# Optimization experiments

Measured on AMD Instinct MI355X. Metric: run time of the kernel, lower is better.

## Reference

```python
import jax, jax.numpy as jnp
import numpy as np

B = 32768
IN_DIM, OUT_DIM, VAR_DIM = 2, 3, 50
KER_DIMS = [1024, 1024, 1024, 1024]
NSTEPS = 32  # fixed-step RK4 stand-in for adaptive odeint over t in [0, 1]


def setup_inputs() -> dict:
    key = jax.random.key(0)
    ks = jax.random.split(key, 11)
    x = jax.random.normal(ks[0], (B, IN_DIM), dtype=jnp.float32)
    dims = [VAR_DIM] + KER_DIMS + [VAR_DIM]
    inp = {"x": x}
    for i, (d1, d2) in enumerate(zip(dims[:-1], dims[1:])):
        # torch Linear(d1+1, d2): weight (d2, d1+1); stored here as (d1+1, d2)
        bound = 1.0 / np.sqrt(d1 + 1)
        inp[f"W{i}"] = jax.random.uniform(ks[1 + 2 * i], (d1 + 1, d2), jnp.float32, -bound, bound)
        inp[f"b{i}"] = jax.random.uniform(ks[2 + 2 * i], (d2,), jnp.float32, -bound, bound)
    return inp


def _odefunc(t, y, Ws, bs):
    # Each layer: concat time column, Linear, ReLU (except last) -- matches ODEfunc.forward
    out = y
    n = len(Ws)
    for i in range(n):
        tcol = jnp.full((out.shape[0], 1), t, dtype=out.dtype)
        h = jnp.concatenate([out, tcol], axis=1)
        out = h @ Ws[i] + bs[i]
        if i < n - 1:
            out = jax.nn.relu(out)
    return out


def _integrate(x, Ws, bs):
    # Pad input into var_dim state: out[:, :in_dim] = x, rest zeros
    y0 = jnp.zeros((x.shape[0], VAR_DIM), dtype=x.dtype).at[:, : x.shape[1]].set(x)
    dt = jnp.asarray(1.0 / NSTEPS, dtype=x.dtype)
    ts = jnp.arange(NSTEPS, dtype=x.dtype) * dt

    def step(y, t):
        k1 = _odefunc(t, y, Ws, bs)
        k2 = _odefunc(t + dt * 0.5, y + dt * 0.5 * k1, Ws, bs)
        k3 = _odefunc(t + dt * 0.5, y + dt * 0.5 * k2, Ws, bs)
        k4 = _odefunc(t + dt, y + dt * k3, Ws, bs)
        return y + (dt / 6.0) * (k1 + 2.0 * k2 + 2.0 * k3 + k4), None

    y1, _ = jax.lax.scan(step, y0, ts)
    return y1[:, :OUT_DIM]


def reference(x, W0, b0, W1, b1, W2, b2, W3, b3, W4, b4):
    Ws = (W0, W1, W2, W3, W4)
    bs = (b0, b1, b2, b3, b4)
    return _integrate(x, Ws, bs)
```

## Files before the change

kernel.cpp:

```cpp
#include <hip/hip_runtime.h>
#include <hip/hip_bf16.h>
#include <stdint.h>


typedef __bf16 bf16_t;
typedef bf16_t bf16x8 __attribute__((ext_vector_type(8)));
typedef float  f32x4  __attribute__((ext_vector_type(4)));

#define DEVI static __device__ __forceinline__

DEVI void gload_lds16(const bf16_t* gsrc, bf16_t* ldst) {
  __builtin_amdgcn_global_load_lds(
      (const __attribute__((address_space(1))) uint32_t*)gsrc,
      (__attribute__((address_space(3))) uint32_t*)ldst,
      16, 0, 0);
}

template<int K>
__global__ __launch_bounds__(512, 2) void gemm256(
    const bf16_t* __restrict__ A,
    const bf16_t* __restrict__ BT,
    const float* __restrict__ bias,
    const float* __restrict__ wtime,
    float t,
    bf16_t* __restrict__ C, int ldc,
    int M, int N)
{
  constexpr int NT = K / 64;
  static_assert(NT >= 2, "need >=2 K-tiles");

  __shared__ __align__(16) bf16_t As[2][256][64];
  __shared__ __align__(16) bf16_t Bs[2][256][64];

  const int tid  = threadIdx.x;
  const int wave = tid >> 6;
  const int lane = tid & 63;
  const int wr = wave >> 2;
  const int wc = wave & 3;

  int wg = blockIdx.x;
  {
    const int cpx = gridDim.x >> 3;
    wg = (wg & 7) * cpx + (wg >> 3);
  }
  const int nbn = N >> 8;
  const int bm = (wg / nbn) << 8;
  const int bn = (wg % nbn) << 8;

  const int srow = lane >> 3;
  const int scol = ((lane & 7) << 3) ^ ((lane & 32) >> 1);
  const bf16_t* aS = A  + (size_t)(bm + wave * 8 + srow) * K + scol;
  const bf16_t* bS = BT + (size_t)(bn + wave * 8 + srow) * K + scol;
  bf16_t* aD = &As[0][0][0] + wave * 8 * 64;
  bf16_t* bD = &Bs[0][0][0] + wave * 8 * 64;

  auto stage = [&](int g) {
    if (g >= 4 * NT) return;
    const int kt   = g >> 2;
    const int idx  = g & 3;
    const int hoff = (idx >> 1) << 7;
    const int buf  = kt & 1;
    const bf16_t* src = (idx & 1) ? bS : aS;
    bf16_t*       dst = (idx & 1) ? bD : aD;
    src += (size_t)hoff * K + kt * 64;
    dst += (buf * 256 + hoff) * 64;
    gload_lds16(src,                dst);
    gload_lds16(src + (size_t)64*K, dst + 64 * 64);
  };

  const int fr = lane & 15;
  const int fq = lane >> 4;

  bf16x8 af[8];
  bf16x8 bfr[8];
  f32x4  acc[8][4] = {};

  auto lda_frag = [&](int buf, int mh) {
    const char* base = (const char*)&As[buf][0][0];
#pragma unroll
    for (int m = 0; m < 4; ++m)
#pragma unroll
      for (int kk = 0; kk < 2; ++kk) {
        int r  = wr * 128 + (mh * 4 + m) * 16 + fr;
        int cb = (kk * 64 + fq * 16) ^ ((r & 4) << 3);
        af[m * 2 + kk] = *(const bf16x8*)(base + r * 128 + cb);
      }
  };
  auto ldb_frag = [&](int buf, int nh) {
    const char* base = (const char*)&Bs[buf][0][0];
#pragma unroll
    for (int n = 0; n < 2; ++n)
#pragma unroll
      for (int kk = 0; kk < 2; ++kk) {
        int r  = wc * 64 + (nh * 2 + n) * 16 + fr;
        int cb = (kk * 64 + fq * 16) ^ ((r & 4) << 3);
        bfr[nh * 4 + n * 2 + kk] = *(const bf16x8*)(base + r * 128 + cb);
      }
  };
  auto mma_quad = [&](int mh, int nh) {
    __builtin_amdgcn_s_setprio(1);
#pragma unroll
    for (int m = 0; m < 4; ++m)
#pragma unroll
      for (int n = 0; n < 2; ++n)
#pragma unroll
        for (int kk = 0; kk < 2; ++kk)
          acc[mh * 4 + m][nh * 2 + n] = __builtin_amdgcn_mfma_f32_16x16x32_bf16(
              af[m * 2 + kk], bfr[nh * 4 + n * 2 + kk],
              acc[mh * 4 + m][nh * 2 + n], 0, 0, 0);
    __builtin_amdgcn_s_setprio(0);
  };

#pragma unroll
  for (int g = 0; g < 7; ++g) stage(g);
  asm volatile("s_waitcnt vmcnt(6)" ::: "memory");
  __builtin_amdgcn_s_barrier();

  for (int t2 = 0; t2 < NT; ++t2) {
    const int buf = t2 & 1;
    const int gb  = t2 * 4 + 7;
    lda_frag(buf, 0);
    ldb_frag(buf, 0);
    stage(gb + 0);
    asm volatile("s_waitcnt lgkmcnt(8)" ::: "memory");
    __builtin_amdgcn_s_barrier();
    asm volatile("s_waitcnt lgkmcnt(0)" ::: "memory");
    mma_quad(0, 0);
    __builtin_amdgcn_s_barrier();
    ldb_frag(buf, 1);
    stage(gb + 1);
    __builtin_amdgcn_s_barrier();
    asm volatile("s_waitcnt lgkmcnt(0)" ::: "memory");
    mma_quad(0, 1);
    __builtin_amdgcn_s_barrier();
    lda_frag(buf, 1);
    stage(gb + 2);
    __builtin_amdgcn_s_barrier();
    asm volatile("s_waitcnt lgkmcnt(0)" ::: "memory");
    mma_quad(1, 0);
    __builtin_amdgcn_s_barrier();
    stage(gb + 3);
    if (t2 < NT - 2) asm volatile("s_waitcnt vmcnt(6)" ::: "memory");
    else             asm volatile("s_waitcnt vmcnt(0)" ::: "memory");
    __builtin_amdgcn_s_barrier();
    mma_quad(1, 1);
    __builtin_amdgcn_s_barrier();
  }

#pragma unroll
  for (int n = 0; n < 4; ++n) {
    const int gcol = bn + wc * 64 + n * 16 + fr;
    const float bv = bias[gcol] + t * wtime[gcol];
#pragma unroll
    for (int m = 0; m < 8; ++m) {
      const int grow0 = bm + wr * 128 + m * 16 + (fq << 2);
#pragma unroll
      for (int r = 0; r < 4; ++r) {
        float v = acc[m][n][r] + bv;
        v = v > 0.0f ? v : 0.0f;
        C[(size_t)(grow0 + r) * ldc + gcol] = (bf16_t)v;
      }
    }
  }
}

template<int BM, int BN, int BK, int WROWS, int WCOLS, bool RELU, bool OUT_BF16>
__global__ __launch_bounds__(256) void gemm_bt(
    const bf16_t* __restrict__ A, int lda,
    const bf16_t* __restrict__ BT,
    const float* __restrict__ bias,
    const float* __restrict__ wtime,
    float t,
    void* __restrict__ Cv, int ldc,
    int M, int K)
{
  constexpr int MR  = BM / WROWS / 16;
  constexpr int NR  = BN / WCOLS / 16;
  constexpr int TPR = BK / 8;
  constexpr int RPW = 64 / TPR;
  constexpr int RPL = 4 * RPW;
  static_assert(BM % RPL == 0 && BN % RPL == 0, "tile staging mismatch");

  __shared__ bf16_t As[BM][BK];
  __shared__ bf16_t Bs[BN][BK];

  const int tid  = threadIdx.x;
  const int wave = tid >> 6;
  const int lane = tid & 63;
  const int wr = wave / WCOLS;
  const int wc = wave % WCOLS;
  const int bm = blockIdx.x * BM;
  const int bn = blockIdx.y * BN;
  const int lrow = lane / TPR;
  const int lcol = (lane % TPR) * 8;

  f32x4 acc[MR][NR] = {};

  for (int k0 = 0; k0 < K; k0 += BK) {
#pragma unroll
    for (int i = 0; i < BM / RPL; ++i) {
      const int rb = i * RPL + wave * RPW;
      gload_lds16(&A[(size_t)(bm + rb + lrow) * lda + k0 + lcol], &As[rb][0]);
    }
#pragma unroll
    for (int i = 0; i < BN / RPL; ++i) {
      const int rb = i * RPL + wave * RPW;
      gload_lds16(&BT[(size_t)(bn + rb + lrow) * K + k0 + lcol], &Bs[rb][0]);
    }
    __syncthreads();
#pragma unroll
    for (int kk = 0; kk < BK / 32; ++kk) {
      bf16x8 af[MR], bfr[NR];
#pragma unroll
      for (int m = 0; m < MR; ++m)
        af[m] = *(const bf16x8*)&As[wr * (BM / WROWS) + m * 16 + (lane & 15)]
                                  [kk * 32 + (lane >> 4) * 8];
#pragma unroll
      for (int n = 0; n < NR; ++n)
        bfr[n] = *(const bf16x8*)&Bs[wc * (BN / WCOLS) + n * 16 + (lane & 15)]
                                    [kk * 32 + (lane >> 4) * 8];
#pragma unroll
      for (int m = 0; m < MR; ++m)
#pragma unroll
        for (int n = 0; n < NR; ++n)
          acc[m][n] = __builtin_amdgcn_mfma_f32_16x16x32_bf16(
              af[m], bfr[n], acc[m][n], 0, 0, 0);
    }
    __syncthreads();
  }

#pragma unroll
  for (int n = 0; n < NR; ++n) {
    const int gcol = bn + wc * (BN / WCOLS) + n * 16 + (lane & 15);
    const float bv = bias[gcol] + t * wtime[gcol];
#pragma unroll
    for (int m = 0; m < MR; ++m) {
      const int grow0 = bm + wr * (BM / WROWS) + m * 16 + ((lane >> 4) << 2);
#pragma unroll
      for (int r = 0; r < 4; ++r) {
        float v = acc[m][n][r] + bv;
        if (RELU) v = v > 0.0f ? v : 0.0f;
        if constexpr (OUT_BF16)
          ((bf16_t*)Cv)[(size_t)(grow0 + r) * ldc + gcol] = (bf16_t)v;
        else
          ((float*)Cv)[(size_t)(grow0 + r) * ldc + gcol] = v;
      }
    }
  }
}

__global__ __launch_bounds__(256) void gemm_l4_rk4(
    const bf16_t* __restrict__ A, int lda,
    const bf16_t* __restrict__ BT,
    const float* __restrict__ bias,
    const float* __restrict__ wtime,
    float t,
    float* __restrict__ y, float* __restrict__ accb,
    bf16_t* __restrict__ ybf,
    float ca, float cs, int mode,
    int M, int K)
{
  constexpr int BM = 128, BN = 64, BK = 64;
  constexpr int MR = 4, NR = 2;

  __shared__ bf16_t As[BM][BK];
  __shared__ bf16_t Bs[BN][BK];

  const int tid  = threadIdx.x;
  const int wave = tid >> 6;
  const int lane = tid & 63;
  const int wr = wave >> 1;
  const int wc = wave & 1;
  const int bm = blockIdx.x * BM;
  const int lrow = lane >> 3;
  const int lcol = (lane & 7) * 8;

  f32x4 acc[MR][NR] = {};

  for (int k0 = 0; k0 < K; k0 += BK) {
#pragma unroll
    for (int i = 0; i < 4; ++i) {
      const int rb = i * 32 + wave * 8;
      gload_lds16(&A[(size_t)(bm + rb + lrow) * lda + k0 + lcol], &As[rb][0]);
    }
#pragma unroll
    for (int i = 0; i < 2; ++i) {
      const int rb = i * 32 + wave * 8;
      gload_lds16(&BT[(size_t)(rb + lrow) * K + k0 + lcol], &Bs[rb][0]);
    }
    __syncthreads();
#pragma unroll
    for (int kk = 0; kk < 2; ++kk) {
      bf16x8 af[MR], bfr[NR];
#pragma unroll
      for (int m = 0; m < MR; ++m)
        af[m] = *(const bf16x8*)&As[wr * 64 + m * 16 + (lane & 15)]
                                  [kk * 32 + (lane >> 4) * 8];
#pragma unroll
      for (int n = 0; n < NR; ++n)
        bfr[n] = *(const bf16x8*)&Bs[wc * 32 + n * 16 + (lane & 15)]
                                    [kk * 32 + (lane >> 4) * 8];
#pragma unroll
      for (int m = 0; m < MR; ++m)
#pragma unroll
        for (int n = 0; n < NR; ++n)
          acc[m][n] = __builtin_amdgcn_mfma_f32_16x16x32_bf16(
              af[m], bfr[n], acc[m][n], 0, 0, 0);
    }
    __syncthreads();
  }

#pragma unroll
  for (int n = 0; n < NR; ++n) {
    const int gcol = wc * 32 + n * 16 + (lane & 15);
    const float bv = bias[gcol] + t * wtime[gcol];
#pragma unroll
    for (int m = 0; m < MR; ++m) {
      const int grow0 = bm + wr * 64 + m * 16 + ((lane >> 4) << 2);
#pragma unroll
      for (int r = 0; r < 4; ++r) {
        const float kv = acc[m][n][r] + bv;
        const size_t o = (size_t)(grow0 + r) * 64 + gcol;
        if (mode == 0) {
          accb[o] = kv;
          ybf[o] = (bf16_t)(y[o] + cs * kv);
        } else if (mode == 1) {
          accb[o] += ca * kv;
          ybf[o] = (bf16_t)(y[o] + cs * kv);
        } else {
          const float ny = y[o] + cs * (accb[o] + kv);
          y[o] = ny;
          ybf[o] = (bf16_t)ny;
        }
      }
    }
  }
}

__global__ void prep_weight(const float* __restrict__ W, const float* __restrict__ b,
                            bf16_t* __restrict__ WT, float* __restrict__ bias,
                            float* __restrict__ wtime,
                            int K, int N, int Kpad, int Npad)
{
  int idx = blockIdx.x * 256 + threadIdx.x;
  int total = Npad * Kpad;
  if (idx < total) {
    int n = idx / Kpad, k = idx % Kpad;
    float v = (n < N && k < K) ? W[(size_t)k * N + n] : 0.0f;
    WT[idx] = (bf16_t)v;
  }
  if (idx < Npad) {
    bias[idx]  = (idx < N) ? b[idx] : 0.0f;
    wtime[idx] = (idx < N) ? W[(size_t)K * N + idx] : 0.0f;
  }
}

__global__ void init_y(const float* __restrict__ x, float* __restrict__ y,
                       bf16_t* __restrict__ ybf, int M)
{
  int i = blockIdx.x * 256 + threadIdx.x;
  if (i < M * 64) {
    int m = i >> 6, c = i & 63;
    float v = (c < 2) ? x[m * 2 + c] : 0.0f;
    y[i] = v;
    ybf[i] = (bf16_t)v;
  }
}

__global__ void extract_out(const float* __restrict__ y, float* __restrict__ out, int M)
{
  int i = blockIdx.x * 256 + threadIdx.x;
  if (i < M * 3) {
    int m = i / 3, c = i % 3;
    out[i] = y[(size_t)m * 64 + c];
  }
}

extern "C" void kernel_launch(void* const* d_in, const int* in_sizes, int n_in,
                              void* d_out, int out_size, void* d_ws, size_t ws_size,
                              hipStream_t stream)
{
  (void)in_sizes; (void)n_in; (void)out_size; (void)ws_size;
  const int M = 32768;

  const float* x = (const float*)d_in[0];
  const float* Wp[5]; const float* bp[5];
  for (int i = 0; i < 5; ++i) {
    Wp[i] = (const float*)d_in[1 + 2 * i];
    bp[i] = (const float*)d_in[2 + 2 * i];
  }

  char* ws = (char*)d_ws; size_t off = 0;
  auto alloc = [&](size_t bytes) -> char* {
    char* p = ws + off; off += (bytes + 255) & ~(size_t)255; return p;
  };

  bf16_t* WT[5];
  WT[0] = (bf16_t*)alloc((size_t)1024 * 64 * 2);
  WT[1] = (bf16_t*)alloc((size_t)1024 * 1024 * 2);
  WT[2] = (bf16_t*)alloc((size_t)1024 * 1024 * 2);
  WT[3] = (bf16_t*)alloc((size_t)1024 * 1024 * 2);
  WT[4] = (bf16_t*)alloc((size_t)64 * 1024 * 2);
  float* bias[5]; float* wtm[5];
  for (int i = 0; i < 5; ++i) {
    int Np = (i == 4) ? 64 : 1024;
    bias[i] = (float*)alloc((size_t)Np * 4);
    wtm[i]  = (float*)alloc((size_t)Np * 4);
  }
  float*  y    = (float*)alloc((size_t)M * 64 * 4);
  float*  accb = (float*)alloc((size_t)M * 64 * 4);
  bf16_t* ybf  = (bf16_t*)alloc((size_t)M * 64 * 2);
  bf16_t* act0 = (bf16_t*)alloc((size_t)M * 1024 * 2);
  bf16_t* act1 = (bf16_t*)alloc((size_t)M * 1024 * 2);

  const int Kd[5]  = {50, 1024, 1024, 1024, 1024};
  const int Nd[5]  = {1024, 1024, 1024, 1024, 50};
  const int Kpd[5] = {64, 1024, 1024, 1024, 1024};
  const int Npd[5] = {1024, 1024, 1024, 1024, 64};
  for (int i = 0; i < 5; ++i) {
    int tot = Npd[i] * Kpd[i];
    prep_weight<<<dim3((tot + 255) / 256), 256, 0, stream>>>(
        Wp[i], bp[i], WT[i], bias[i], wtm[i], Kd[i], Nd[i], Kpd[i], Npd[i]);
  }

  init_y<<<dim3((M * 64 + 255) / 256), 256, 0, stream>>>(x, y, ybf, M);

  const float dtv = 1.0f / 32.0f;
  dim3 gL0(M / 128, 1024 / 128);
  dim3 g256(M / 256 * (1024 / 256));
  dim3 gL4(M / 128);

  auto run_net = [&](float t, float ca, float cs, int mode) {
    gemm_bt<128,128,64,2,2,true,true><<<gL0, 256, 0, stream>>>(
        ybf, 64, WT[0], bias[0], wtm[0], t, act0, 1024, M, 64);
    gemm256<1024><<<g256, 512, 0, stream>>>(
        act0, WT[1], bias[1], wtm[1], t, act1, 1024, M, 1024);
    gemm256<1024><<<g256, 512, 0, stream>>>(
        act1, WT[2], bias[2], wtm[2], t, act0, 1024, M, 1024);
    gemm256<1024><<<g256, 512, 0, stream>>>(
        act0, WT[3], bias[3], wtm[3], t, act1, 1024, M, 1024);
    gemm_l4_rk4<<<gL4, 256, 0, stream>>>(
        act1, 1024, WT[4], bias[4], wtm[4], t,
        y, accb, ybf, ca, cs, mode, M, 1024);
  };

  for (int i = 0; i < 32; ++i) {
    const float t0 = i * dtv;
    const float tm = t0 + 0.5f * dtv;
    const float t1 = t0 + dtv;
    run_net(t0, 0.0f, 0.5f * dtv, 0);
    run_net(tm, 2.0f, 0.5f * dtv, 1);
    run_net(tm, 2.0f, dtv,        1);
    run_net(t1, 0.0f, dtv / 6.0f, 2);
  }

  extract_out<<<dim3((M * 3 + 255) / 256), 256, 0, stream>>>(y, (float*)d_out, M);
}
```

Before: 40.94 ms.

## Reorder gemm256 prefetch to stage next tile halves earlier; shrink L4 tile to 64 rows

The staging schedule in the 256x256 GEMM is reworked so that within each k-iteration the upper halves of the next tile and the lower halves of the tile after that are loaded, with a vmcnt(4) wait instead of the old 7-deep staged sequence. Loads can then be issued ahead of need in a different order and memory waits may shorten. Separately, the final 1024->64 layer kernel drops from 128 to 64 rows per block, doubling the block count so more CUs stay busy. The new wait counts must match the outstanding loads exactly, otherwise LDS reads could race.

```diff
diff --git a/kernel.cpp b/kernel.cpp
--- a/kernel.cpp
+++ b/kernel.cpp
@@ -54,18 +54,12 @@
   bf16_t* aD = &As[0][0][0] + wave * 8 * 64;
   bf16_t* bD = &Bs[0][0][0] + wave * 8 * 64;
 
-  auto stage = [&](int g) {
-    if (g >= 4 * NT) return;
-    const int kt   = g >> 2;
-    const int idx  = g & 3;
-    const int hoff = (idx >> 1) << 7;
-    const int buf  = kt & 1;
-    const bf16_t* src = (idx & 1) ? bS : aS;
-    bf16_t*       dst = (idx & 1) ? bD : aD;
-    src += (size_t)hoff * K + kt * 64;
-    dst += (buf * 256 + hoff) * 64;
-    gload_lds16(src,                dst);
-    gload_lds16(src + (size_t)64*K, dst + 64 * 64);
+  auto stageHalf = [&](int kt, int isB, int h) {
+    const int buf = kt & 1;
+    const bf16_t* src = (isB ? bS : aS) + (size_t)(h * 128) * K + kt * 64;
+    bf16_t*       dst = (isB ? bD : aD) + (buf * 256 + h * 128) * 64;
+    gload_lds16(src,                 dst);
+    gload_lds16(src + (size_t)64 * K, dst + 64 * 64);
   };
 
   const int fr = lane & 15;
@@ -111,37 +105,40 @@
     __builtin_amdgcn_s_setprio(0);
   };
 
-#pragma unroll
-  for (int g = 0; g < 7; ++g) stage(g);
-  asm volatile("s_waitcnt vmcnt(6)" ::: "memory");
+  stageHalf(0, 0, 0); stageHalf(0, 1, 0);
+  stageHalf(0, 0, 1); stageHalf(0, 1, 1);
+  stageHalf(1, 1, 0); stageHalf(1, 0, 0);
+  asm volatile("s_waitcnt vmcnt(4)" ::: "memory");
   __builtin_amdgcn_s_barrier();
 
   for (int t2 = 0; t2 < NT; ++t2) {
     const int buf = t2 & 1;
-    const int gb  = t2 * 4 + 7;
     lda_frag(buf, 0);
     ldb_frag(buf, 0);
-    stage(gb + 0);
+    if (t2 + 1 < NT) stageHalf(t2 + 1, 0, 1);
     asm volatile("s_waitcnt lgkmcnt(8)" ::: "memory");
     __builtin_amdgcn_s_barrier();
     asm volatile("s_waitcnt lgkmcnt(0)" ::: "memory");
     mma_quad(0, 0);
     __builtin_amdgcn_s_barrier();
     ldb_frag(buf, 1);
-    stage(gb + 1);
+    if (t2 + 1 < NT) stageHalf(t2 + 1, 1, 1);
     __builtin_amdgcn_s_barrier();
     asm volatile("s_waitcnt lgkmcnt(0)" ::: "memory");
     mma_quad(0, 1);
     __builtin_amdgcn_s_barrier();
     lda_frag(buf, 1);
-    stage(gb + 2);
+    if (t2 + 2 < NT) stageHalf(t2 + 2, 1, 0);
     __builtin_amdgcn_s_barrier();
     asm volatile("s_waitcnt lgkmcnt(0)" ::: "memory");
     mma_quad(1, 0);
     __builtin_amdgcn_s_barrier();
-    stage(gb + 3);
-    if (t2 < NT - 2) asm volatile("s_waitcnt vmcnt(6)" ::: "memory");
-    else             asm volatile("s_waitcnt vmcnt(0)" ::: "memory");
+    if (t2 + 2 < NT) {
+      stageHalf(t2 + 2, 0, 0);
+      asm volatile("s_waitcnt vmcnt(4)" ::: "memory");
+    } else {
+      asm volatile("s_waitcnt vmcnt(0)" ::: "memory");
+    }
     __builtin_amdgcn_s_barrier();
     mma_quad(1, 1);
     __builtin_amdgcn_s_barrier();
@@ -260,8 +257,8 @@
     float ca, float cs, int mode,
     int M, int K)
 {
-  constexpr int BM = 128, BN = 64, BK = 64;
-  constexpr int MR = 4, NR = 2;
+  constexpr int BM = 64, BN = 64, BK = 64;
+  constexpr int MR = 2, NR = 2;
 
   __shared__ bf16_t As[BM][BK];
   __shared__ bf16_t Bs[BN][BK];
@@ -279,7 +276,7 @@
 
   for (int k0 = 0; k0 < K; k0 += BK) {
 #pragma unroll
-    for (int i = 0; i < 4; ++i) {
+    for (int i = 0; i < 2; ++i) {
       const int rb = i * 32 + wave * 8;
       gload_lds16(&A[(size_t)(bm + rb + lrow) * lda + k0 + lcol], &As[rb][0]);
     }
@@ -294,7 +291,7 @@
       bf16x8 af[MR], bfr[NR];
 #pragma unroll
       for (int m = 0; m < MR; ++m)
-        af[m] = *(const bf16x8*)&As[wr * 64 + m * 16 + (lane & 15)]
+        af[m] = *(const bf16x8*)&As[wr * 32 + m * 16 + (lane & 15)]
                                   [kk * 32 + (lane >> 4) * 8];
 #pragma unroll
       for (int n = 0; n < NR; ++n)
@@ -316,7 +313,7 @@
     const float bv = bias[gcol] + t * wtime[gcol];
 #pragma unroll
     for (int m = 0; m < MR; ++m) {
-      const int grow0 = bm + wr * 64 + m * 16 + ((lane >> 4) << 2);
+      const int grow0 = bm + wr * 32 + m * 16 + ((lane >> 4) << 2);
 #pragma unroll
       for (int r = 0; r < 4; ++r) {
         const float kv = acc[m][n][r] + bv;
@@ -428,7 +425,7 @@
   const float dtv = 1.0f / 32.0f;
   dim3 gL0(M / 128, 1024 / 128);
   dim3 g256(M / 256 * (1024 / 256));
-  dim3 gL4(M / 128);
+  dim3 gL4(M / 64);
 
   auto run_net = [&](float t, float ca, float cs, int mode) {
     gemm_bt<128,128,64,2,2,true,true><<<gL0, 256, 0, stream>>>(
```

Result: faster. 39.60 ms (-3.3%).
